# Kernel optimization log

Measured on AMD Instinct MI355X. Metric: run time of the kernel, lower is better.

The kernel has to match this reference:

```python
import jax, jax.numpy as jnp
from jax import lax
import numpy as np

DIM, K, OUT_DIM = 128, 64, 256
SAMPLE_STEP = 30  # eval mode
WIN = 200


def _l2n(v, axis):
    return v / jnp.maximum(jnp.linalg.norm(v, axis=axis, keepdims=True), 1e-12)


def _conv(x, w, b, pad):
    y = lax.conv_general_dilated(x, w, (1, 1), [(pad, pad), (pad, pad)],
                                 dimension_numbers=('NCHW', 'OIHW', 'NCHW'))
    return y + b[None, :, None, None]


def _maxpool(x, kh, kw, sh, sw, ph, pw):
    return lax.reduce_window(x, -jnp.inf, lax.max, (1, 1, kh, kw), (1, 1, sh, sw),
                             [(0, 0), (0, 0), (ph, ph), (pw, pw)])


def setup_inputs() -> dict:
    key = jax.random.key(0)
    ks = jax.random.split(key, 12)
    s = 1.0 / np.sqrt(DIM)
    return {
        'x': jax.random.normal(ks[0], (4, DIM, 48, 900), jnp.float32),
        'cluster_centers': jax.random.uniform(ks[1], (K, DIM), jnp.float32) * s,
        'conv_w': jax.random.normal(ks[2], (K, DIM), jnp.float32) * s * 0.1,
        'conv_b': jax.random.normal(ks[3], (K,), jnp.float32) * s * 0.1,
        'w1': jax.random.normal(ks[4], (2 * DIM, DIM, 5, 5), jnp.float32) * 0.02,
        'b1': jnp.zeros((2 * DIM,), jnp.float32),
        'w2': jax.random.normal(ks[5], (4 * DIM, 2 * DIM, 5, 5), jnp.float32) * 0.01,
        'b2': jnp.zeros((4 * DIM,), jnp.float32),
        'w3': jax.random.normal(ks[6], (8 * DIM, 4 * DIM, 5, 5), jnp.float32) * 0.01,
        'b3': jnp.zeros((8 * DIM,), jnp.float32),
        'mlp_w': jax.random.normal(ks[7], (OUT_DIM, DIM * (K + 8)), jnp.float32) * s * 0.01,
        'mlp_b': jax.random.normal(ks[8], (OUT_DIM,), jnp.float32) * s * 0.01,
    }


def reference(x, cluster_centers, conv_w, conv_b, w1, b1, w2, b2, w3, b3, mlp_w, mlp_b):
    N, C, H, W = x.shape  # (4, 128, 48, 900)
    # ---- soft assignment (1x1 conv), softmax over clusters ----
    logits = jnp.einsum('nchw,kc->nkhw', x, conv_w) + conv_b[None, :, None, None]
    a = jax.nn.softmax(logits, axis=1)  # softmax over K (per spatial pos)
    # ---- residual-weighted sum over H, fused (avoids (N,K,C,HW) tensor) ----
    # sum_h a[n,k,h,w] * (x[n,c,h,w] - centers[k,c])
    xa = jnp.einsum('nkhw,nchw->nkcw', a, x)
    a_sum = a.sum(axis=2)  # (N,K,W)
    res = xa - cluster_centers[None, :, :, None] * a_sum[:, :, None, :]  # (N,K,C,W)
    # ---- x_conv feature branch on circularly padded input ----
    xp = jnp.concatenate([x[..., 800:], x, x[..., :100]], axis=-1)  # (N,C,H,1100)
    h = jax.nn.leaky_relu(_conv(xp, w1, b1, 2), 0.2)
    h = _maxpool(h, 3, 3, 3, 1, 0, 1)          # (N,256,16,1100)
    h = jax.nn.leaky_relu(_conv(h, w2, b2, 2), 0.2)
    h = _maxpool(h, 4, 5, 4, 1, 0, 2)          # (N,512,4,1100)
    h = _conv(h, w3, b3, 2)
    h = _maxpool(h, 4, WIN, 4, 1, 0, 0)        # (N,1024,1,901)
    xf = h[:, :, 0, ::SAMPLE_STEP][..., :-1]   # (N,1024,30)
    xf = _l2n(jnp.transpose(xf, (0, 2, 1)), axis=2)  # (N,30,1024)
    n_win = xf.shape[1]
    # ---- windowed VLAD pooling via cumsum (equiv to unfold(200, step).sum) ----
    resp = jnp.concatenate([res[..., 800:], res, res[..., :100]], axis=-1)  # (N,K,C,1100)
    cs = jnp.concatenate([jnp.zeros_like(resp[..., :1]), jnp.cumsum(resp, axis=-1)], axis=-1)
    starts = jnp.arange(n_win) * SAMPLE_STEP  # last window dropped, matching [:-1]
    vlad = cs[..., starts + WIN] - cs[..., starts]  # (N,K,C,30)
    vlad = jnp.transpose(vlad, (0, 3, 1, 2))        # (N,30,K,C)
    vlad = _l2n(vlad, axis=3)                        # intra-norm per cluster
    vlad = _l2n(vlad.reshape(N * n_win, K * C), axis=1)
    feat = jnp.concatenate([vlad, xf.reshape(N * n_win, -1)], axis=1)  # (N*30, 9216)
    out = _l2n(feat @ mlp_w.T + mlp_b, axis=1)
    return out.reshape(N, n_win, -1)
```

## Files before the change

kernel.cpp:

```cpp
#include <hip/hip_runtime.h>
#include <hip/hip_bf16.h>

#define NB   4
#define DIM  128
#define KC   64
#define HH   48
#define WW   900
#define WPAD 1100
#define WST  1160
#define NT   30
#define OC1  256
#define OC2  512
#define OC3  1024

typedef __attribute__((ext_vector_type(8))) short bf16x8;
typedef __attribute__((ext_vector_type(4))) float f32x4;
typedef unsigned short u16;
typedef unsigned int u32;

__device__ __forceinline__ u16 f2bf(float f){
  __hip_bfloat16 h = __float2bfloat16(f);
  u16 u; __builtin_memcpy(&u, &h, 2); return u;
}
__device__ __forceinline__ float bf2f(u16 u){
  __hip_bfloat16 h; __builtin_memcpy(&h, &u, 2); return __bfloat162float(h);
}

typedef __attribute__((address_space(1))) const u32 g_u32;
typedef __attribute__((address_space(3))) u32 l_u32;
__device__ __forceinline__ void gll16(const void* g, void* l){
  __builtin_amdgcn_global_load_lds((g_u32*)g, (l_u32*)l, 16, 0, 0);
}


__global__ __launch_bounds__(256) void transpose_xt(const float* __restrict__ x, float* __restrict__ xt){
  __shared__ float tile[32][33];
  int n = blockIdx.z;
  int r0 = blockIdx.y*32, w0 = blockIdx.x*32;
  int t = threadIdx.x;
  int tr = t >> 5, tc = t & 31;
  #pragma unroll
  for (int i = 0; i < 4; ++i){
    int r = r0 + tr + i*8, w = w0 + tc;
    tile[tr + i*8][tc] = (w < WW) ? x[((size_t)n*(DIM*HH) + r)*WW + w] : 0.f;
  }
  __syncthreads();
  #pragma unroll
  for (int i = 0; i < 4; ++i){
    int w = w0 + tr + i*8, r = r0 + tc;
    if (w < WW) xt[((size_t)n*WW + w)*(DIM*HH) + r] = tile[tc][tr + i*8];
  }
}

__global__ __launch_bounds__(256) void vlad_softmax(const float* __restrict__ x,
    const float* __restrict__ conv_w, const float* __restrict__ conv_b, float* __restrict__ a){
  __shared__ float cwT[DIM*KC];
  __shared__ float cbs[KC];
  int t = threadIdx.x;
  for (int i = t; i < DIM*KC; i += 256){ int c = i >> 6, k = i & 63; cwT[i] = conv_w[k*DIM + c]; }
  if (t < KC) cbs[t] = conv_b[t];
  __syncthreads();
  int w = blockIdx.x*256 + t, h = blockIdx.y, n = blockIdx.z;
  bool ok = (w < WW);
  float lg[KC];
  #pragma unroll
  for (int k = 0; k < KC; ++k) lg[k] = cbs[k];
  const float* xp = x + (size_t)n*DIM*HH*WW + (size_t)h*WW + (ok ? w : 0);
  for (int c = 0; c < DIM; ++c){
    float xv = ok ? xp[(size_t)c*HH*WW] : 0.f;
    const float* cw = &cwT[c*KC];
    #pragma unroll
    for (int k = 0; k < KC; ++k) lg[k] += xv * cw[k];
  }
  float m = lg[0];
  #pragma unroll
  for (int k = 1; k < KC; ++k) m = fmaxf(m, lg[k]);
  float s = 0.f;
  #pragma unroll
  for (int k = 0; k < KC; ++k){ lg[k] = __expf(lg[k]-m); s += lg[k]; }
  float inv = 1.f/s;
  if (ok){
    float* dst = a + (((size_t)(n*HH + h))*WW + w)*KC;
    #pragma unroll
    for (int k = 0; k < KC; k += 4){
      float4 v = make_float4(lg[k]*inv, lg[k+1]*inv, lg[k+2]*inv, lg[k+3]*inv);
      *(float4*)&dst[k] = v;
    }
  }
}

__global__ __launch_bounds__(256) void vlad_xa2(const float* __restrict__ xt, const float* __restrict__ a,
    const float* __restrict__ centers, float* __restrict__ ps){
  __shared__ float aT[HH][KC];
  __shared__ float xT[DIM*HH];
  int t = threadIdx.x, s = blockIdx.x, n = blockIdx.y;
  int k = t >> 2, cb4 = t & 3;
  float acc[32];
  #pragma unroll
  for (int j = 0; j < 32; ++j) acc[j] = 0.f;
  float Sacc = 0.f;
  for (int i = 0; i < 10; ++i){
    int p = s*10 + i;
    int w = (p < 100) ? p + 800 : ((p < 1000) ? p - 100 : p - 1000);
    for (int e = t; e < HH*KC; e += 256){
      int h = e >> 6, kk = e & 63;
      aT[h][kk] = a[(((size_t)(n*HH + h))*WW + w)*KC + kk];
    }
    {
      const float4* src = (const float4*)(xt + ((size_t)n*WW + w)*(DIM*HH));
      float4* dst4 = (float4*)xT;
      for (int e = t; e < (DIM*HH)/4; e += 256) dst4[e] = src[e];
    }
    __syncthreads();
    float areg[HH];
    #pragma unroll
    for (int h = 0; h < HH; ++h) areg[h] = aT[h][k];
    float Sw = 0.f;
    #pragma unroll
    for (int h = 0; h < HH; ++h) Sw += areg[h];
    Sacc += Sw;
    #pragma unroll 2
    for (int j = 0; j < 32; ++j){
      const float4* xr = (const float4*)&xT[(cb4 + 4*j)*HH];
      float sum = 0.f;
      #pragma unroll
      for (int h4 = 0; h4 < HH/4; ++h4){
        float4 xv = xr[h4];
        sum += areg[h4*4+0]*xv.x + areg[h4*4+1]*xv.y + areg[h4*4+2]*xv.z + areg[h4*4+3]*xv.w;
      }
      acc[j] += sum;
    }
    __syncthreads();
  }
  const float* ck = centers + (size_t)k*DIM;
  float* dst = ps + (((size_t)(n*KC + k))*110 + s)*DIM;
  #pragma unroll
  for (int j = 0; j < 32; ++j){
    int c = cb4 + 4*j;
    dst[c] = acc[j] - ck[c]*Sacc;
  }
}

__global__ __launch_bounds__(128) void vlad_win2(const float* __restrict__ ps, float* __restrict__ vlad){
  int c = threadIdx.x, k = blockIdx.x, tt = blockIdx.y, n = blockIdx.z;
  const float* base = ps + ((size_t)(n*KC + k))*110*DIM + c;
  float v = 0.f;
  #pragma unroll
  for (int u = 0; u < 20; ++u) v += base[(3*tt + u)*DIM];
  float ss = v*v;
  #pragma unroll
  for (int m = 1; m < 64; m <<= 1) ss += __shfl_xor(ss, m);
  __shared__ float red[2];
  if ((c & 63) == 0) red[c >> 6] = ss;
  __syncthreads();
  float tot = red[0] + red[1];
  float inv = 1.f / fmaxf(sqrtf(tot), 1e-12f);
  vlad[(((size_t)(n*NT + tt))*KC + k)*DIM + c] = v*inv;
}

__global__ __launch_bounds__(256) void vlad_gnorm(float* __restrict__ vlad){
  int row = blockIdx.x, t = threadIdx.x;
  float4* v = (float4*)(vlad + (size_t)row*(KC*DIM));
  float4 r[8]; float ss = 0.f;
  #pragma unroll
  for (int i = 0; i < 8; ++i){
    r[i] = v[t + i*256];
    ss += r[i].x*r[i].x + r[i].y*r[i].y + r[i].z*r[i].z + r[i].w*r[i].w;
  }
  #pragma unroll
  for (int m = 1; m < 64; m <<= 1) ss += __shfl_xor(ss, m);
  __shared__ float red[4];
  if ((t & 63) == 0) red[t >> 6] = ss;
  __syncthreads();
  float tot = red[0]+red[1]+red[2]+red[3];
  float inv = 1.f / fmaxf(sqrtf(tot), 1e-12f);
  #pragma unroll
  for (int i = 0; i < 8; ++i){
    float4 o = r[i]; o.x*=inv; o.y*=inv; o.z*=inv; o.w*=inv;
    v[t + i*256] = o;
  }
}


__global__ __launch_bounds__(256) void build_xpb(const float* __restrict__ x, u16* __restrict__ xpb){
  __shared__ u16 tile[DIM][33];
  int t = threadIdx.x, h = blockIdx.y, n = blockIdx.z;
  int b0 = blockIdx.x*32;
  #pragma unroll
  for (int i = 0; i < 16; ++i){
    int e = t + i*256;
    int c = e >> 5, bl = e & 31;
    int b = b0 + bl, w = b - 2;
    float v = 0.f;
    if (w >= 0 && w < WPAD){
      int wsrc = (w + 800) % 900;
      v = x[((size_t)(n*DIM + c)*HH + h)*WW + wsrc];
    }
    tile[c][bl] = f2bf(v);
  }
  __syncthreads();
  #pragma unroll
  for (int i = 0; i < 16; ++i){
    int e = t + i*256;
    int bl = e >> 7, c = e & 127;
    int b = b0 + bl;
    if (b < WST) xpb[((size_t)(n*HH + h)*WST + b)*DIM + c] = tile[c][bl];
  }
}

__global__ __launch_bounds__(256) void pack_w2(const float* __restrict__ w, u16* __restrict__ wp,
    int OC, int IC, int NICB){
  int idx = blockIdx.x*256 + threadIdx.x;
  int total = OC*IC*25;
  if (idx >= total) return;
  int e = idx & 7;
  int q = idx >> 3;
  int oc = q % OC;  int q2 = q / OC;
  int lgp = q2 & 3; int k0i = (q2 >> 2) & 3;
  int q3 = q2 >> 4;
  int icb = q3 % NICB; int tap = q3 / NICB;
  int ic = icb*128 + k0i*32 + lgp*8 + e;
  wp[idx] = f2bf(w[((size_t)oc*IC + ic)*25 + tap]);
}

template<int IC, int OC, int H>
__global__ __launch_bounds__(256,2) void conv5x5(const u16* __restrict__ in, const u16* __restrict__ wp,
    const float* __restrict__ bias, u16* __restrict__ out){
  constexpr int NICB = IC/128;
  constexpr int LN = (NICB==1?0:(NICB==2?1:2));
  __shared__ u16 sIn[2][132*128];
  int t = threadIdx.x;
  int wave = t >> 6, lane = t & 63, lr = lane & 15, lgp = lane >> 4;
  int w0  = blockIdx.x * 128;
  int ocb = blockIdx.y * 256;
  int nh = blockIdx.z; int n = nh / H, h = nh % H;
  int wo_oc = wave*64;
  f32x4 acc[4][8] = {};
  const u16* inN = in + (size_t)n*H*WST*IC;
  const size_t laneA = (size_t)(ocb + wo_oc + lr)*8;
  int dhlo = (2-h > 0) ? (2-h) : 0;
  int dhhi = (H+1-h < 4) ? (H+1-h) : 4;
  int nslab = (dhhi - dhlo + 1) << LN;

  auto stage = [&](int slab_, int buf_){
    int dh = dhlo + (slab_ >> LN);
    int icb = slab_ & (NICB-1);
    const u16* rowbase = inN + (size_t)(h + dh - 2)*WST*IC + (size_t)icb*128;
    for (int i = wave; i < 33; i += 4){
      int qq = i*64 + lane;
      int r = qq >> 4, cp = qq & 15;
      int c = cp ^ (r & 7);
      gll16(rowbase + (size_t)(w0 + r)*IC + c*8, &sIn[buf_][i*512]);
    }
  };

  stage(0, 0);
  __syncthreads();

  for (int slab = 0; slab < nslab; ++slab){
    int buf = slab & 1;
    if (slab + 1 < nslab) stage(slab + 1, buf ^ 1);
    int dh = dhlo + (slab >> LN);
    int icb = slab & (NICB-1);
    const u16* wslab = wp + (size_t)(dh*5*NICB + icb)*16*OC*8 + laneA;
    const u16* sB = &sIn[buf][0];
    bf16x8 Abuf[3][4];
    #pragma unroll
    for (int pi = 0; pi < 2; ++pi){
      const u16* ap = wslab + (size_t)((pi >> 2)*NICB*16 + ((pi & 3)*4 + lgp))*OC*8;
      #pragma unroll
      for (int ja = 0; ja < 4; ++ja) Abuf[pi][ja] = *(const bf16x8*)(ap + (size_t)ja*16*8);
    }
    #pragma unroll
    for (int dw = 0; dw < 5; ++dw){
      #pragma unroll
      for (int k0i = 0; k0i < 4; ++k0i){
        constexpr int NI = 20;
        const int i = dw*4 + k0i;
        {
          const int pn = (i + 2 < NI) ? (i + 2) : (NI - 1);
          const u16* ap = wslab + (size_t)((pn >> 2)*NICB*16 + ((pn & 3)*4 + lgp))*OC*8;
          #pragma unroll
          for (int ja = 0; ja < 4; ++ja) Abuf[(i + 2) % 3][ja] = *(const bf16x8*)(ap + (size_t)ja*16*8);
        }
        bf16x8 B[8];
        #pragma unroll
        for (int jb = 0; jb < 8; ++jb){
          int br = jb*16 + lr + dw;
          B[jb] = *(const bf16x8*)&sB[br*128 + (((k0i*4 + lgp) ^ (br & 7)) << 3)];
        }
        __builtin_amdgcn_s_setprio(1);
        #pragma unroll
        for (int ja = 0; ja < 4; ++ja)
          #pragma unroll
          for (int jb = 0; jb < 8; ++jb)
            acc[ja][jb] = __builtin_amdgcn_mfma_f32_16x16x32_bf16(Abuf[i % 3][ja], B[jb], acc[ja][jb], 0, 0, 0);
        __builtin_amdgcn_s_setprio(0);
      }
    }
    __syncthreads();
  }

  u16* outP = out + ((size_t)(n*H + h)*WST + 2)*OC;
  #pragma unroll
  for (int ja = 0; ja < 4; ++ja){
    int oc = ocb + wo_oc + ja*16 + lgp*4;
    float4 bv = *(const float4*)&bias[oc];
    #pragma unroll
    for (int jb = 0; jb < 8; ++jb){
      int wg = w0 + jb*16 + lr;
      if (wg < WPAD){
        f32x4 av = acc[ja][jb];
        ushort4 o;
        o.x = f2bf(av[0] + bv.x);
        o.y = f2bf(av[1] + bv.y);
        o.z = f2bf(av[2] + bv.z);
        o.w = f2bf(av[3] + bv.w);
        *(ushort4*)(outP + (size_t)wg*OC + oc) = o;
      }
    }
  }
}

__global__ __launch_bounds__(256) void pool1k(const u16* __restrict__ in, u16* __restrict__ out){
  int t = threadIdx.x;
  int wb = blockIdx.x*4 + (t >> 6);
  int oc = (t & 63)*4;
  int ho = blockIdx.y, n = blockIdx.z;
  int wo = wb - 2;
  float m0=0.f,m1=0.f,m2=0.f,m3=0.f;
  if (wo >= 0 && wo < WPAD){
    m0=m1=m2=m3=-1e30f;
    #pragma unroll
    for (int kh = 0; kh < 3; ++kh){
      const u16* row = in + ((size_t)(n*HH + ho*3 + kh)*WST + 2)*OC1 + oc;
      #pragma unroll
      for (int kw = 0; kw < 3; ++kw){
        int wi = wo - 1 + kw;
        if (wi >= 0 && wi < WPAD){
          ushort4 v = *(const ushort4*)(row + (size_t)wi*OC1);
          m0 = fmaxf(m0, bf2f(v.x)); m1 = fmaxf(m1, bf2f(v.y));
          m2 = fmaxf(m2, bf2f(v.z)); m3 = fmaxf(m3, bf2f(v.w));
        }
      }
    }
    m0 = (m0>0.f)?m0:0.2f*m0; m1 = (m1>0.f)?m1:0.2f*m1;
    m2 = (m2>0.f)?m2:0.2f*m2; m3 = (m3>0.f)?m3:0.2f*m3;
  }
  ushort4 o; o.x=f2bf(m0); o.y=f2bf(m1); o.z=f2bf(m2); o.w=f2bf(m3);
  *(ushort4*)(out + ((size_t)(n*16 + ho)*WST + wb)*OC1 + oc) = o;
}

__global__ __launch_bounds__(256) void pool2k(const u16* __restrict__ in, u16* __restrict__ out){
  int t = threadIdx.x;
  int wb = blockIdx.x*2 + (t >> 7);
  int oc = (t & 127)*4;
  int ho = blockIdx.y, n = blockIdx.z;
  int wo = wb - 2;
  float m0=0.f,m1=0.f,m2=0.f,m3=0.f;
  if (wo >= 0 && wo < WPAD){
    m0=m1=m2=m3=-1e30f;
    #pragma unroll
    for (int kh = 0; kh < 4; ++kh){
      const u16* row = in + ((size_t)(n*16 + ho*4 + kh)*WST + 2)*OC2 + oc;
      #pragma unroll
      for (int kw = 0; kw < 5; ++kw){
        int wi = wo - 2 + kw;
        if (wi >= 0 && wi < WPAD){
          ushort4 v = *(const ushort4*)(row + (size_t)wi*OC2);
          m0 = fmaxf(m0, bf2f(v.x)); m1 = fmaxf(m1, bf2f(v.y));
          m2 = fmaxf(m2, bf2f(v.z)); m3 = fmaxf(m3, bf2f(v.w));
        }
      }
    }
    m0 = (m0>0.f)?m0:0.2f*m0; m1 = (m1>0.f)?m1:0.2f*m1;
    m2 = (m2>0.f)?m2:0.2f*m2; m3 = (m3>0.f)?m3:0.2f*m3;
  }
  ushort4 o; o.x=f2bf(m0); o.y=f2bf(m1); o.z=f2bf(m2); o.w=f2bf(m3);
  *(ushort4*)(out + ((size_t)(n*4 + ho)*WST + wb)*OC2 + oc) = o;
}

__global__ __launch_bounds__(256) void pool3k(const u16* __restrict__ in, float* __restrict__ xfraw){
  int tt = blockIdx.x, hh = blockIdx.y, n = blockIdx.z;
  int oc = threadIdx.x*4;
  float m0=-1e30f,m1=-1e30f,m2=-1e30f,m3=-1e30f;
  const u16* row = in + ((size_t)(n*4 + hh)*WST + 2 + 30*tt)*OC3 + oc;
  for (int p = 0; p < 200; ++p){
    ushort4 v = *(const ushort4*)(row + (size_t)p*OC3);
    m0 = fmaxf(m0, bf2f(v.x)); m1 = fmaxf(m1, bf2f(v.y));
    m2 = fmaxf(m2, bf2f(v.z)); m3 = fmaxf(m3, bf2f(v.w));
  }
  float* dst = xfraw + (((size_t)(n*NT + tt))*4 + hh)*OC3 + oc;
  dst[0]=m0; dst[1]=m1; dst[2]=m2; dst[3]=m3;
}

__global__ __launch_bounds__(256) void xf_norm(const float* __restrict__ xfraw, float* __restrict__ xf){
  int row = blockIdx.x, t = threadIdx.x;
  const float* src = xfraw + (size_t)row*4096;
  float v[4]; float ss = 0.f;
  #pragma unroll
  for (int j = 0; j < 4; ++j){
    float m = src[t + j*256];
    #pragma unroll
    for (int hh = 1; hh < 4; ++hh) m = fmaxf(m, src[hh*1024 + t + j*256]);
    v[j] = m; ss += m*m;
  }
  #pragma unroll
  for (int m = 1; m < 64; m <<= 1) ss += __shfl_xor(ss, m);
  __shared__ float red[4];
  if ((t & 63) == 0) red[t >> 6] = ss;
  __syncthreads();
  float tot = red[0]+red[1]+red[2]+red[3];
  float inv = 1.f/fmaxf(sqrtf(tot), 1e-12f);
  float* dst = xf + (size_t)row*OC3;
  #pragma unroll
  for (int j = 0; j < 4; ++j) dst[t + j*256] = v[j]*inv;
}

__global__ __launch_bounds__(256) void mlp_part(const float* __restrict__ vlad, const float* __restrict__ xf,
    const float* __restrict__ W, float* __restrict__ part){
  __shared__ float feat[4][256];
  int kc = blockIdx.x, rb = blockIdx.y, t = threadIdx.x;
  int i0 = kc*256;
  #pragma unroll
  for (int r = 0; r < 4; ++r){
    int row = rb*4 + r;
    int i = i0 + t;
    feat[r][t] = (i < 8192) ? vlad[(size_t)row*8192 + i] : xf[(size_t)row*1024 + (i - 8192)];
  }
  __syncthreads();
  const float* wr = W + (size_t)t*9216 + i0;
  float a0=0.f, a1=0.f, a2=0.f, a3=0.f;
  for (int i = 0; i < 256; i += 4){
    float4 wv = *(const float4*)&wr[i];
    a0 += feat[0][i]*wv.x + feat[0][i+1]*wv.y + feat[0][i+2]*wv.z + feat[0][i+3]*wv.w;
    a1 += feat[1][i]*wv.x + feat[1][i+1]*wv.y + feat[1][i+2]*wv.z + feat[1][i+3]*wv.w;
    a2 += feat[2][i]*wv.x + feat[2][i+1]*wv.y + feat[2][i+2]*wv.z + feat[2][i+3]*wv.w;
    a3 += feat[3][i]*wv.x + feat[3][i+1]*wv.y + feat[3][i+2]*wv.z + feat[3][i+3]*wv.w;
  }
  float* p0 = part + (((size_t)(rb*4 + 0)*36 + kc))*256 + t;
  p0[0]          = a0;
  p0[36*256]     = a1;
  p0[2*36*256]   = a2;
  p0[3*36*256]   = a3;
}

__global__ __launch_bounds__(256) void mlp_reduce(const float* __restrict__ part, const float* __restrict__ b,
    float* __restrict__ out){
  int row = blockIdx.x, t = threadIdx.x;
  const float* pr = part + (size_t)row*36*256 + t;
  float acc = b[t];
  #pragma unroll
  for (int kc = 0; kc < 36; ++kc) acc += pr[kc*256];
  float ss = acc*acc;
  #pragma unroll
  for (int m = 1; m < 64; m <<= 1) ss += __shfl_xor(ss, m);
  __shared__ float red[4];
  if ((t & 63) == 0) red[t >> 6] = ss;
  __syncthreads();
  float tot = red[0]+red[1]+red[2]+red[3];
  float inv = 1.f/fmaxf(sqrtf(tot), 1e-12f);
  out[(size_t)row*256 + t] = acc*inv;
}

extern "C" void kernel_launch(void* const* d_in, const int* in_sizes, int n_in,
                              void* d_out, int out_size, void* d_ws, size_t ws_size,
                              hipStream_t stream){
  const float* x       = (const float*)d_in[0];
  const float* centers = (const float*)d_in[1];
  const float* conv_w  = (const float*)d_in[2];
  const float* conv_b  = (const float*)d_in[3];
  const float* w1      = (const float*)d_in[4];
  const float* b1      = (const float*)d_in[5];
  const float* w2      = (const float*)d_in[6];
  const float* b2      = (const float*)d_in[7];
  const float* w3      = (const float*)d_in[8];
  const float* b3      = (const float*)d_in[9];
  const float* mlp_w   = (const float*)d_in[10];
  const float* mlp_b   = (const float*)d_in[11];
  float* out = (float*)d_out;
  char* ws = (char*)d_ws;
  const size_t MB = 1ull << 20;
  if (ws_size < 248*MB) return;

  float* vlad  = (float*)(ws + 0);
  float* xf    = (float*)(ws + 4*MB);
  float* xfraw = (float*)(ws + 5*MB);
  char*  AR    = ws + 7*MB;
  float* xt = (float*)(AR + 0);
  float* a  = (float*)(AR + 85*MB);
  float* ps = (float*)(AR + 128*MB);
  u16* xpb = (u16*)(AR + 0);
  u16* wp1 = (u16*)(AR + 55*MB);
  u16* wp2 = (u16*)(AR + 57*MB);
  u16* wp3 = (u16*)(AR + 64*MB);
  u16* h1  = (u16*)(AR + 89*MB);
  u16* p1  = (u16*)(AR + 0);
  u16* h2  = (u16*)(AR + 89*MB);
  u16* p2  = (u16*)(AR + 163*MB);
  u16* h3  = (u16*)(AR + 0);
  float* part = (float*)(AR + 200*MB);

  transpose_xt<<<dim3(29,192,NB), 256, 0, stream>>>(x, xt);
  vlad_softmax<<<dim3(4,HH,NB), 256, 0, stream>>>(x, conv_w, conv_b, a);
  vlad_xa2<<<dim3(110,NB), 256, 0, stream>>>(xt, a, centers, ps);
  vlad_win2<<<dim3(KC,NT,NB), 128, 0, stream>>>(ps, vlad);
  vlad_gnorm<<<dim3(NB*NT), 256, 0, stream>>>(vlad);

  pack_w2<<<dim3(3200),  256, 0, stream>>>(w1, wp1, OC1, DIM, 1);
  pack_w2<<<dim3(12800), 256, 0, stream>>>(w2, wp2, OC2, OC1, 2);
  pack_w2<<<dim3(51200), 256, 0, stream>>>(w3, wp3, OC3, OC2, 4);
  build_xpb<<<dim3(37,HH,NB), 256, 0, stream>>>(x, xpb);
  conv5x5<128,256,48><<<dim3(9, OC1/256, NB*HH), 256, 0, stream>>>(xpb, wp1, b1, h1);
  pool1k<<<dim3(WST/4,16,NB), 256, 0, stream>>>(h1, p1);
  conv5x5<256,512,16><<<dim3(9, OC2/256, NB*16), 256, 0, stream>>>(p1, wp2, b2, h2);
  pool2k<<<dim3(WST/2,4,NB), 256, 0, stream>>>(h2, p2);
  conv5x5<512,1024,4><<<dim3(9, OC3/256, NB*4), 256, 0, stream>>>(p2, wp3, b3, h3);
  pool3k<<<dim3(NT,4,NB), 256, 0, stream>>>(h3, xfraw);
  xf_norm<<<dim3(NB*NT), 256, 0, stream>>>(xfraw, xf);

  mlp_part<<<dim3(36,30), 256, 0, stream>>>(vlad, xf, mlp_w, part);
  mlp_reduce<<<dim3(NB*NT), 256, 0, stream>>>(part, mlp_b, out);
}
```

Before: 1.636 ms.

## Drop x transpose and stream x directly into VLAD accumulation with double buffering

Removes the transpose_xt kernel, which wrote a full transposed copy of x (about 88 MB). The VLAD aggregation kernel now reads x in its native layout, loading one h row for 10 w positions per step into double-buffered shared memory, and accumulates over h as an outer loop. This saves the extra read and write pass over x. In exchange, the global loads of x are strided across channels (10 contiguous floats per row), there are 48 barrier-synchronised iterations per block, and a single launch of 440 blocks may hide latency poorly.

```diff
diff --git a/kernel.cpp b/kernel.cpp
--- a/kernel.cpp
+++ b/kernel.cpp
@@ -33,25 +33,6 @@
 }
 
 
-__global__ __launch_bounds__(256) void transpose_xt(const float* __restrict__ x, float* __restrict__ xt){
-  __shared__ float tile[32][33];
-  int n = blockIdx.z;
-  int r0 = blockIdx.y*32, w0 = blockIdx.x*32;
-  int t = threadIdx.x;
-  int tr = t >> 5, tc = t & 31;
-  #pragma unroll
-  for (int i = 0; i < 4; ++i){
-    int r = r0 + tr + i*8, w = w0 + tc;
-    tile[tr + i*8][tc] = (w < WW) ? x[((size_t)n*(DIM*HH) + r)*WW + w] : 0.f;
-  }
-  __syncthreads();
-  #pragma unroll
-  for (int i = 0; i < 4; ++i){
-    int w = w0 + tr + i*8, r = r0 + tc;
-    if (w < WW) xt[((size_t)n*WW + w)*(DIM*HH) + r] = tile[tc][tr + i*8];
-  }
-}
-
 __global__ __launch_bounds__(256) void vlad_softmax(const float* __restrict__ x,
     const float* __restrict__ conv_w, const float* __restrict__ conv_b, float* __restrict__ a){
   __shared__ float cwT[DIM*KC];
@@ -89,55 +70,65 @@
   }
 }
 
-__global__ __launch_bounds__(256) void vlad_xa2(const float* __restrict__ xt, const float* __restrict__ a,
+__global__ __launch_bounds__(256) void vlad_xa3(const float* __restrict__ x, const float* __restrict__ a,
     const float* __restrict__ centers, float* __restrict__ ps){
-  __shared__ float aT[HH][KC];
-  __shared__ float xT[DIM*HH];
+  __shared__ float xw[2][10][132];
+  __shared__ float aw[2][10][64];
   int t = threadIdx.x, s = blockIdx.x, n = blockIdx.y;
   int k = t >> 2, cb4 = t & 3;
+  int p0 = s*10;
+  int w0 = (p0 < 100) ? p0 + 800 : ((p0 < 1000) ? p0 - 100 : p0 - 1000);
+  const float* xn = x + (size_t)n*DIM*HH*WW + w0;
+  const float* an = a + (size_t)n*HH*WW*KC + (size_t)w0*KC;
+
+  auto load = [&](int h, int buf){
+    if (t < 128){
+      const float* xr = xn + ((size_t)t*HH + h)*WW;
+      #pragma unroll
+      for (int w = 0; w < 10; ++w) xw[buf][w][t] = xr[w];
+    } else {
+      const float* ar = an + (size_t)h*WW*KC;
+      int e0 = (t - 128)*5;
+      #pragma unroll
+      for (int q = 0; q < 5; ++q){ int e = e0 + q; aw[buf][e >> 6][e & 63] = ar[e]; }
+    }
+  };
+
   float acc[32];
   #pragma unroll
   for (int j = 0; j < 32; ++j) acc[j] = 0.f;
   float Sacc = 0.f;
-  for (int i = 0; i < 10; ++i){
-    int p = s*10 + i;
-    int w = (p < 100) ? p + 800 : ((p < 1000) ? p - 100 : p - 1000);
-    for (int e = t; e < HH*KC; e += 256){
-      int h = e >> 6, kk = e & 63;
-      aT[h][kk] = a[(((size_t)(n*HH + h))*WW + w)*KC + kk];
-    }
-    {
-      const float4* src = (const float4*)(xt + ((size_t)n*WW + w)*(DIM*HH));
-      float4* dst4 = (float4*)xT;
-      for (int e = t; e < (DIM*HH)/4; e += 256) dst4[e] = src[e];
-    }
+
+  load(0, 0);
+  for (int h = 0; h < HH; ++h){
+    int buf = h & 1;
     __syncthreads();
-    float areg[HH];
-    #pragma unroll
-    for (int h = 0; h < HH; ++h) areg[h] = aT[h][k];
-    float Sw = 0.f;
-    #pragma unroll
-    for (int h = 0; h < HH; ++h) Sw += areg[h];
-    Sacc += Sw;
+    if (h + 1 < HH) load(h + 1, buf ^ 1);
     #pragma unroll 2
-    for (int j = 0; j < 32; ++j){
-      const float4* xr = (const float4*)&xT[(cb4 + 4*j)*HH];
-      float sum = 0.f;
-      #pragma unroll
-      for (int h4 = 0; h4 < HH/4; ++h4){
-        float4 xv = xr[h4];
-        sum += areg[h4*4+0]*xv.x + areg[h4*4+1]*xv.y + areg[h4*4+2]*xv.z + areg[h4*4+3]*xv.w;
+    for (int w = 0; w < 10; ++w){
+      float av = aw[buf][w][k];
+      Sacc += av;
+      const float4* xr4 = (const float4*)&xw[buf][w][cb4*32];
+      #pragma unroll
+      for (int jj = 0; jj < 8; ++jj){
+        float4 xv = xr4[jj];
+        acc[jj*4+0] += av*xv.x; acc[jj*4+1] += av*xv.y;
+        acc[jj*4+2] += av*xv.z; acc[jj*4+3] += av*xv.w;
       }
-      acc[j] += sum;
     }
     __syncthreads();
   }
-  const float* ck = centers + (size_t)k*DIM;
-  float* dst = ps + (((size_t)(n*KC + k))*110 + s)*DIM;
-  #pragma unroll
-  for (int j = 0; j < 32; ++j){
-    int c = cb4 + 4*j;
-    dst[c] = acc[j] - ck[c]*Sacc;
+
+  const float* ck = centers + (size_t)k*DIM + cb4*32;
+  float* dst = ps + (((size_t)(n*KC + k))*110 + s)*DIM + cb4*32;
+  #pragma unroll
+  for (int jj = 0; jj < 8; ++jj){
+    float4 o;
+    o.x = acc[jj*4+0] - ck[jj*4+0]*Sacc;
+    o.y = acc[jj*4+1] - ck[jj*4+1]*Sacc;
+    o.z = acc[jj*4+2] - ck[jj*4+2]*Sacc;
+    o.w = acc[jj*4+3] - ck[jj*4+3]*Sacc;
+    *(float4*)&dst[jj*4] = o;
   }
 }
 
@@ -487,7 +478,6 @@
   float* xf    = (float*)(ws + 4*MB);
   float* xfraw = (float*)(ws + 5*MB);
   char*  AR    = ws + 7*MB;
-  float* xt = (float*)(AR + 0);
   float* a  = (float*)(AR + 85*MB);
   float* ps = (float*)(AR + 128*MB);
   u16* xpb = (u16*)(AR + 0);
@@ -501,9 +491,8 @@
   u16* h3  = (u16*)(AR + 0);
   float* part = (float*)(AR + 200*MB);
 
-  transpose_xt<<<dim3(29,192,NB), 256, 0, stream>>>(x, xt);
   vlad_softmax<<<dim3(4,HH,NB), 256, 0, stream>>>(x, conv_w, conv_b, a);
-  vlad_xa2<<<dim3(110,NB), 256, 0, stream>>>(xt, a, centers, ps);
+  vlad_xa3<<<dim3(110,NB), 256, 0, stream>>>(x, a, centers, ps);
   vlad_win2<<<dim3(KC,NT,NB), 128, 0, stream>>>(ps, vlad);
   vlad_gnorm<<<dim3(NB*NT), 256, 0, stream>>>(vlad);
 
```

New measurement: 1.574 ms. 1.04x faster.
